# Kernel optimization log

Hardware: AMD Instinct MI355X
Metric: run time of the kernel (lower is better)

The kernel has to match this reference:

```python
import jax, jax.numpy as jnp
import numpy as np

B, S, D, H, E, K, DH = 4, 1024, 1024, 8, 4, 2, 128


def setup_inputs() -> dict:
    key = jax.random.key(0)
    ks = jax.random.split(key, 9)
    std = 1.0 / np.sqrt(D)
    f = lambda k, shape, s: jax.random.normal(k, shape, dtype=jnp.float32) * s
    return {
        'q_src': f(ks[0], (B, S, D), 1.0),
        'k_src': f(ks[1], (B, S, D), 1.0),
        'v_src': f(ks[2], (B, S, D), 1.0),
        'Wq': f(ks[3], (H * DH, D), std),
        'Wk': f(ks[4], (H * DH, D), std),
        'Wv': f(ks[5], (H * E, D, DH), std),
        'Wo': f(ks[6], (H * E, DH, D), 1.0 / np.sqrt(H * DH)),
        'sel_v': f(ks[7], (H * E, D), std),
        'sel_o': f(ks[8], (H * E, D), std),
    }


def _route(src, selw):
    # sigmoid-gated per-head top-k expert selection (get_sel), eval mode
    g = jax.nn.sigmoid((src @ selw.T).reshape(*src.shape[:-1], H, E))  # [B,S,H,E]
    val, idx = jax.lax.top_k(g, K)
    # dense per-expert mixture weights: zeros except top-k sigmoid gates
    return (jax.nn.one_hot(idx, E, dtype=g.dtype) * val[..., None]).sum(-2)  # [B,S,H,E]


def reference(q_src, k_src, v_src, Wq, Wk, Wv, Wo, sel_v, sel_o):
    scale = (1.0 / np.sqrt(DH)) ** 0.5  # scale.sqrt() applied to both q and k
    q = ((q_src @ Wq.T) * scale).reshape(B, S, H, DH).transpose(0, 2, 1, 3)  # [B,H,S,DH]
    k = ((k_src @ Wk.T) * scale).reshape(B, S, H, DH).transpose(0, 2, 1, 3)

    wv = _route(k_src, sel_v)  # [B,S,H,E] V-expert gates (from keys)
    wo = _route(q_src, sel_o)  # [B,S,H,E] O-expert gates (from queries)

    # cvmm V: per-token top-k mixture of expert V projections
    v_all = jnp.einsum('bsd,hedc->bshec', v_src, Wv.reshape(H, E, D, DH))
    v = jnp.einsum('bshec,bshe->bhsc', v_all, wv)  # [B,H,S,DH]

    att = jax.nn.softmax(jnp.einsum('bhqc,bhkc->bhqk', q, k), axis=-1)
    res = jnp.einsum('bhqk,bhkc->bqhc', att, v)  # [B,S,H,DH]

    # cvmm O: weight per-head outputs by gates, project and sum over heads/experts
    resw = res[..., None, :] * wo[..., None]  # [B,S,H,E,DH]
    out = jnp.einsum('bshec,hecd->bsd', resw, Wo.reshape(H, E, DH, D))
    return out
```

## Files before the change

kernel.cpp:

```cpp
#include <hip/hip_runtime.h>

#define DEV __device__ __forceinline__

typedef __attribute__((ext_vector_type(8))) short s8v;
typedef __attribute__((ext_vector_type(4))) short s4v;
typedef __attribute__((ext_vector_type(4))) float f4v;

DEV unsigned short f2b(float f){
    unsigned u = __float_as_uint(f);
    u = (u + 0x7FFFu + ((u >> 16) & 1u)) >> 16;
    return (unsigned short)u;
}
DEV float b2f(short s){ return __uint_as_float(((unsigned)(unsigned short)s) << 16); }

DEV void gload16(const void* g, void* l){
    __builtin_amdgcn_global_load_lds(
        (const __attribute__((address_space(1))) unsigned*)g,
        (__attribute__((address_space(3))) unsigned*)l, 16, 0, 0);
}


DEV void stage2(const short* A, const short* B, int sA, int sB, int kA, int kB,
                short* la, short* lb, int w, int lane){
    int srow = lane >> 3;
    int swcol = ((lane & 7) ^ srow) << 3;
    #pragma unroll
    for(int it = 0; it < 4; it++){
        int seg = (w << 2) + it;
        int row = (seg << 3) + srow;
        gload16(&A[(size_t)row * sA + kA + swcol], &la[seg << 9]);
        gload16(&B[(size_t)row * sB + kB + swcol], &lb[seg << 9]);
    }
}

DEV void mfma_block(const short* la, const short* lb, int wm, int wn, int qr, int grp, f4v acc[4][4]){
    #pragma unroll
    for(int ks = 0; ks < 2; ks++){
        s8v af[4], bf[4];
        #pragma unroll
        for(int m = 0; m < 4; m++)
            af[m] = *(const s8v*)&la[(wm + m * 16 + qr) * 64 + ((((ks << 2) + grp) ^ (qr & 7)) << 3)];
        #pragma unroll
        for(int n = 0; n < 4; n++)
            bf[n] = *(const s8v*)&lb[(wn + n * 16 + qr) * 64 + ((((ks << 2) + grp) ^ (qr & 7)) << 3)];
        #pragma unroll
        for(int m = 0; m < 4; m++)
            #pragma unroll
            for(int n = 0; n < 4; n++)
                acc[m][n] = __builtin_amdgcn_mfma_f32_16x16x32_bf16(af[m], bf[n], acc[m][n], 0, 0, 0);
    }
}

__global__ __launch_bounds__(256) void k_cvt(const float* s0, const float* s1, const float* s2,
                                             const float* s3, const float* s4,
                                             short* o0, short* o1, short* o2, short* o3, short* o4){
    int y = blockIdx.y;
    const float* s = (y == 0) ? s0 : (y == 1) ? s1 : (y == 2) ? s2 : (y == 3) ? s3 : s4;
    short* o = (y == 0) ? o0 : (y == 1) ? o1 : (y == 2) ? o2 : (y == 3) ? o3 : o4;
    int n8 = (y < 3) ? 524288 : 131072;
    int idx = blockIdx.x * 256 + threadIdx.x;
    if(idx < n8){
        const float4* f = (const float4*)(s + (size_t)idx * 8);
        float4 a = f[0], b = f[1];
        s8v v;
        v[0] = f2b(a.x); v[1] = f2b(a.y); v[2] = f2b(a.z); v[3] = f2b(a.w);
        v[4] = f2b(b.x); v[5] = f2b(b.y); v[6] = f2b(b.z); v[7] = f2b(b.w);
        *(s8v*)(o + (size_t)idx * 8) = v;
    }
}

__global__ __launch_bounds__(256) void k_transpose(const float* in, short* out, int R, int C){
    in  += (size_t)blockIdx.z * R * C;
    out += (size_t)blockIdx.z * R * C;
    __shared__ float t[32][33];
    int c0 = blockIdx.x * 32, r0 = blockIdx.y * 32;
    int tx = threadIdx.x & 31, ty = threadIdx.x >> 5;
    #pragma unroll
    for(int p = 0; p < 4; p++){
        int r = p * 8 + ty;
        t[r][tx] = in[(size_t)(r0 + r) * C + c0 + tx];
    }
    __syncthreads();
    #pragma unroll
    for(int p = 0; p < 4; p++){
        int c = p * 8 + ty;
        out[(size_t)(c0 + c) * R + r0 + tx] = (short)f2b(t[tx][c]);
    }
}

__global__ __launch_bounds__(256) void k_rlogits(const float* qsrc, const float* ksrc,
                                                 const float* selv, const float* selo,
                                                 float* part){
    int which = blockIdx.y;
    const float* src = which ? qsrc : ksrc;
    const float* sel = which ? selo : selv;
    int tt = blockIdx.x >> 3, ks = blockIdx.x & 7;
    int tok0 = tt << 7;
    __shared__ float lsrc[128][36];
    __shared__ float lsel[32][36];
    int tid = threadIdx.x;
    int ts = tid & 31, es = tid >> 5;
    float acc[4][4];
    #pragma unroll
    for(int j = 0; j < 4; j++)
        #pragma unroll
        for(int i = 0; i < 4; i++) acc[j][i] = 0.f;

    #pragma unroll 1
    for(int c = 0; c < 4; c++){
        int k0 = (ks << 7) + (c << 5);
        {
            int row = tid >> 1, half = tid & 1;
            const float4* g = (const float4*)(src + (size_t)(tok0 + row) * 1024 + k0 + half * 16);
            #pragma unroll
            for(int qq = 0; qq < 4; qq++){
                int qw = half * 4 + qq;
                *(float4*)&lsrc[row][((qw + row) & 7) * 4] = g[qq];
            }
        }
        {
            int row = tid >> 3, qw = tid & 7;
            *(float4*)&lsel[row][((qw + row) & 7) * 4] =
                *(const float4*)(sel + (size_t)row * 1024 + k0 + qw * 4);
        }
        __syncthreads();
        #pragma unroll
        for(int q = 0; q < 8; q++){
            float4 sv[4];
            #pragma unroll
            for(int i = 0; i < 4; i++){
                int e = es * 4 + i;
                sv[i] = *(const float4*)&lsel[e][((q + e) & 7) * 4];
            }
            int slot = ((q + ts) & 7) * 4;
            #pragma unroll
            for(int j = 0; j < 4; j++){
                float4 xv = *(const float4*)&lsrc[ts + 32 * j][slot];
                #pragma unroll
                for(int i = 0; i < 4; i++){
                    acc[j][i] = fmaf(xv.x, sv[i].x, acc[j][i]);
                    acc[j][i] = fmaf(xv.y, sv[i].y, acc[j][i]);
                    acc[j][i] = fmaf(xv.z, sv[i].z, acc[j][i]);
                    acc[j][i] = fmaf(xv.w, sv[i].w, acc[j][i]);
                }
            }
        }
        __syncthreads();
    }
    #pragma unroll
    for(int j = 0; j < 4; j++){
        int token = tok0 + ts + 32 * j;
        f4v st;
        #pragma unroll
        for(int i = 0; i < 4; i++) st[i] = acc[j][i];
        *(f4v*)&part[(((size_t)(ks * 2 + which) * 4096) + token) * 32 + es * 4] = st;
    }
}

__global__ __launch_bounds__(256) void k_rfinal(const float* part, float* wvp, float* wop){
    int which = blockIdx.y;
    float* wout = which ? wop : wvp;
    int tid = threadIdx.x;
    int tok = blockIdx.x * 32 + (tid >> 3), h = tid & 7;
    f4v sum = {0.f, 0.f, 0.f, 0.f};
    #pragma unroll
    for(int s = 0; s < 8; s++)
        sum += *(const f4v*)&part[(((size_t)(s * 2 + which) * 4096) + tok) * 32 + h * 4];
    float g[4];
    #pragma unroll
    for(int e = 0; e < 4; e++) g[e] = 1.0f / (1.0f + expf(-sum[e]));
    f4v out;
    #pragma unroll
    for(int e = 0; e < 4; e++){
        int rank = 0;
        #pragma unroll
        for(int j = 0; j < 4; j++)
            rank += (g[j] > g[e]) || (g[j] == g[e] && j < e);
        out[e] = (rank < 2) ? g[e] : 0.0f;
    }
    *(f4v*)&wout[(size_t)tok * 32 + h * 4] = out;
}

__global__ __launch_bounds__(256) void k_count(const float* wv, int* cntv){
    int he = blockIdx.x, tid = threadIdx.x;
    __shared__ int red[256];
    int c = 0;
    #pragma unroll
    for(int p = 0; p < 16; p++)
        c += (wv[(size_t)(p * 256 + tid) * 32 + he] > 0.f) ? 1 : 0;
    red[tid] = c;
    __syncthreads();
    for(int s = 128; s > 0; s >>= 1){
        if(tid < s) red[tid] += red[tid + s];
        __syncthreads();
    }
    if(tid == 0) cntv[he] = red[0];
}

__global__ __launch_bounds__(256) void k_scan(const int* cntv, int* basev, int* descv){
    __shared__ int ntl[33];
    int tid = threadIdx.x;
    if(tid == 0){
        int run = 0;
        for(int he = 0; he < 32; he++){
            ntl[he] = run;
            run += (cntv[he] + 127) >> 7;
        }
        ntl[32] = run;
    }
    __syncthreads();
    if(tid < 32) basev[tid] = ntl[tid] << 7;
    for(int i = tid; i < 544; i += 256){
        int d = -1;
        for(int he = 0; he < 32; he++)
            if(i >= ntl[he] && i < ntl[he + 1]) d = he;
        descv[i] = d;
    }
}

__global__ __launch_bounds__(256) void k_gather(const float* wv, const int* basev,
                                                int* idxv, float* gbufv, int* rpos){
    int he = blockIdx.x, h = he >> 2, e = he & 3;
    int tid = threadIdx.x, lane = tid & 63, w = tid >> 6;
    int base = basev[he];
    __shared__ int wsum[4];
    __shared__ int running;
    if(tid == 0) running = 0;
    __syncthreads();
    #pragma unroll 1
    for(int p = 0; p < 16; p++){
        int t = p * 256 + tid;
        float g = wv[(size_t)t * 32 + he];
        bool sel = g > 0.f;
        unsigned long long m = __ballot(sel);
        int lpref = __popcll(m & ((1ull << lane) - 1ull));
        if(lane == 0) wsum[w] = __popcll(m);
        __syncthreads();
        int rb = running;
        int woff = 0;
        #pragma unroll
        for(int j = 0; j < 4; j++) woff += (j < w) ? wsum[j] : 0;
        if(sel){
            int pos = base + rb + woff + lpref;
            idxv[pos] = t;
            gbufv[pos] = g;
            int slot = 0;
            #pragma unroll
            for(int j = 0; j < 4; j++)
                slot += (j < e && wv[(size_t)t * 32 + h * 4 + j] > 0.f) ? 1 : 0;
            rpos[(size_t)t * 16 + h * 2 + slot] = pos;
        }
        __syncthreads();
        if(tid == 0) running += wsum[0] + wsum[1] + wsum[2] + wsum[3];
        __syncthreads();
    }
    int tot = running;
    int aligned = (tot + 127) & ~127;
    for(int i = tid; i < aligned - tot; i += 256){
        idxv[base + tot + i] = 0;
        gbufv[base + tot + i] = 0.f;
    }
}

__global__ __launch_bounds__(256) void k_gemmg(const short* vsb, const short* wvt,
                                               const int* descv, const int* idxv,
                                               const float* gbufv, short* Cg){
    int he = descv[blockIdx.x];
    if(he < 0) return;
    int row0 = (int)blockIdx.x << 7;
    __shared__ __align__(16) short la[2][8192];
    __shared__ __align__(16) short lb[2][8192];
    __shared__ int lidx[128];
    int tid = threadIdx.x, lane = tid & 63, w = tid >> 6;
    if(tid < 128) lidx[tid] = idxv[row0 + tid];
    __syncthreads();
    int srow = lane >> 3;
    int swcol = ((lane & 7) ^ srow) << 3;
    int arow[4];
    #pragma unroll
    for(int it = 0; it < 4; it++) arow[it] = lidx[(((w << 2) + it) << 3) + srow];
    const short* Bb = wvt + ((size_t)he << 17);
    int wm = (w >> 1) << 6, wn = (w & 1) << 6;
    int qr = lane & 15, grp = lane >> 4;
    f4v acc[4][4];
    #pragma unroll
    for(int m = 0; m < 4; m++)
        #pragma unroll
        for(int n = 0; n < 4; n++) acc[m][n] = f4v{0.f, 0.f, 0.f, 0.f};
    #pragma unroll 1
    for(int t = -1; t < 16; t++){
        int nxt = t + 1;
        if(nxt < 16){
            int buf = nxt & 1, k0 = nxt << 6;
            #pragma unroll
            for(int it = 0; it < 4; it++){
                int seg = (w << 2) + it;
                int row = (seg << 3) + srow;
                gload16(&vsb[(size_t)arow[it] * 1024 + k0 + swcol], &la[buf][seg << 9]);
                gload16(&Bb[(size_t)row * 1024 + k0 + swcol], &lb[buf][seg << 9]);
            }
        }
        if(t >= 0)
            mfma_block(la[t & 1], lb[t & 1], wm, wn, qr, grp, acc);
        __syncthreads();
    }
    #pragma unroll
    for(int m = 0; m < 4; m++){
        int rl = wm + m * 16 + (grp << 2);
        #pragma unroll
        for(int r = 0; r < 4; r++){
            float g = gbufv[row0 + rl + r];
            #pragma unroll
            for(int n = 0; n < 4; n++){
                int col = wn + n * 16 + qr;
                Cg[(size_t)(row0 + rl + r) * 128 + col] = (short)f2b(acc[m][n][r] * g);
            }
        }
    }
}

__global__ __launch_bounds__(256) void k_vcomb(const short* Cg, const int* rpos, short* vtg){
    int bh = blockIdx.y, b = bh >> 3, h = bh & 7;
    int s0 = blockIdx.x * 32;
    __shared__ __align__(16) short t0[32][136];
    __shared__ __align__(16) short t1[32][136];
    __shared__ int rl[32][2];
    int tid = threadIdx.x;
    if(tid < 64){
        int i = tid >> 1, s = tid & 1;
        rl[i][s] = rpos[(size_t)(b * 1024 + s0 + i) * 16 + h * 2 + s];
    }
    __syncthreads();
    #pragma unroll
    for(int p = 0; p < 4; p++){
        int ch = tid + p * 256;
        int i = ch >> 5, slot = (ch >> 4) & 1, c8 = (ch & 15) << 3;
        s8v v = *(const s8v*)&Cg[(size_t)rl[i][slot] * 128 + c8];
        if(slot) *(s8v*)&t1[i][c8] = v;
        else     *(s8v*)&t0[i][c8] = v;
    }
    __syncthreads();
    #pragma unroll
    for(int p = 0; p < 16; p++){
        int idx = tid + p * 256;
        int s = idx & 31, c = idx >> 5;
        float v = b2f(t0[s][c]) + b2f(t1[s][c]);
        vtg[((size_t)bh * 128 + c) * 1024 + s0 + s] = (short)f2b(v);
    }
}

__global__ __launch_bounds__(256) void k_gemmqk(const short* qsb, const short* ksb,
                                                const short* wqb, const short* wkb,
                                                short* qo, short* ko, float scale){
    __shared__ __align__(16) short la[2][8192];
    __shared__ __align__(16) short lb[2][8192];
    int wg = (blockIdx.x & 7) * 64 + (blockIdx.x >> 3);
    int which = wg >> 8, tl = wg & 255;
    int mt = tl >> 3, nt = tl & 7;
    const short* A = (which ? ksb : qsb) + ((size_t)(mt << 7)) * 1024;
    const short* B = (which ? wkb : wqb) + ((size_t)(nt << 7)) * 1024;
    short* out = which ? ko : qo;
    int tid = threadIdx.x, lane = tid & 63, w = tid >> 6;
    int wm = (w >> 1) << 6, wn = (w & 1) << 6;
    int qr = lane & 15, grp = lane >> 4;
    f4v acc[4][4];
    #pragma unroll
    for(int m = 0; m < 4; m++)
        #pragma unroll
        for(int n = 0; n < 4; n++) acc[m][n] = f4v{0.f, 0.f, 0.f, 0.f};
    #pragma unroll 1
    for(int t = -1; t < 16; t++){
        int nxt = t + 1;
        if(nxt < 16)
            stage2(A, B, 1024, 1024, nxt << 6, nxt << 6, la[nxt & 1], lb[nxt & 1], w, lane);
        if(t >= 0)
            mfma_block(la[t & 1], lb[t & 1], wm, wn, qr, grp, acc);
        __syncthreads();
    }
    #pragma unroll
    for(int m = 0; m < 4; m++){
        int rb = (mt << 7) + wm + m * 16 + (grp << 2);
        #pragma unroll
        for(int n = 0; n < 4; n++){
            int col = (nt << 7) + wn + n * 16 + qr;
            #pragma unroll
            for(int r = 0; r < 4; r++)
                out[(size_t)(rb + r) * 1024 + col] = (short)f2b(acc[m][n][r] * scale);
        }
    }
}

__global__ __launch_bounds__(256) void k_gemmo(const short* resw, const short* wot, float* po){
    __shared__ __align__(16) short la[2][8192];
    __shared__ __align__(16) short lb[2][8192];
    int wg = (blockIdx.x & 7) * 64 + (blockIdx.x >> 3);
    int ksp = wg & 1, tile = wg >> 1;
    int mt = tile >> 3, nt = tile & 7;
    const short* A = resw + (size_t)(mt << 7) * 4096 + ksp * 2048;
    const short* B = wot + (size_t)(nt << 7) * 4096 + ksp * 2048;
    int tid = threadIdx.x, lane = tid & 63, w = tid >> 6;
    int wm = (w >> 1) << 6, wn = (w & 1) << 6;
    int qr = lane & 15, grp = lane >> 4;
    f4v acc[4][4];
    #pragma unroll
    for(int m = 0; m < 4; m++)
        #pragma unroll
        for(int n = 0; n < 4; n++) acc[m][n] = f4v{0.f, 0.f, 0.f, 0.f};
    #pragma unroll 1
    for(int t = -1; t < 32; t++){
        int nxt = t + 1;
        if(nxt < 32)
            stage2(A, B, 4096, 4096, nxt << 6, nxt << 6, la[nxt & 1], lb[nxt & 1], w, lane);
        if(t >= 0)
            mfma_block(la[t & 1], lb[t & 1], wm, wn, qr, grp, acc);
        __syncthreads();
    }
    po += (size_t)ksp * 4194304;
    #pragma unroll
    for(int m = 0; m < 4; m++){
        int rb = (mt << 7) + wm + m * 16 + (grp << 2);
        #pragma unroll
        for(int n = 0; n < 4; n++){
            int col = (nt << 7) + wn + n * 16 + qr;
            #pragma unroll
            for(int r = 0; r < 4; r++)
                po[(size_t)(rb + r) * 1024 + col] = acc[m][n][r];
        }
    }
}

__global__ __launch_bounds__(256) void k_red(const float* p0, const float* p1, float* out){
    size_t idx = ((size_t)blockIdx.x * 256 + threadIdx.x) * 4;
    f4v a = *(const f4v*)&p0[idx];
    f4v b = *(const f4v*)&p1[idx];
    f4v s = a + b;
    *(f4v*)&out[idx] = s;
}

__global__ __launch_bounds__(256) void k_attn(const short* qg, const short* kg,
                                              const short* vtg, short* res){
    __shared__ __align__(16) short lk[2][8192];
    __shared__ __align__(16) short lv[2][8192];
    __shared__ __align__(16) short pl[4][16 * 72];
    int bh = blockIdx.y, b = bh >> 3, h = bh & 7;
    int w = threadIdx.x >> 6, lane = threadIdx.x & 63;
    int qr = lane & 15, grp = lane >> 4;
    int q0 = blockIdx.x * 64 + w * 16;
    const short* vtb = vtg + ((size_t)bh << 17);
    short* pw = &pl[w][0];

    int tok = b * 1024 + q0 + qr;
    s8v qf[4];
    #pragma unroll
    for(int ks = 0; ks < 4; ks++)
        qf[ks] = *(const s8v*)&qg[(size_t)tok * 1024 + h * 128 + ks * 32 + grp * 8];
    f4v o[8];
    #pragma unroll
    for(int ct = 0; ct < 8; ct++) o[ct] = f4v{0.f, 0.f, 0.f, 0.f};
    float m_cur = -1e30f, l_cur = 0.f;

    int klr = lane >> 4, klc = lane & 15;
    int vlr = lane >> 3, vlc = lane & 7;

    #pragma unroll 1
    for(int t = -1; t < 16; t++){
        int nxt = t + 1;
        if(nxt < 16){
            int buf = nxt & 1, kv0 = nxt << 6;
            #pragma unroll
            for(int i = 0; i < 4; i++){
                int seg = (w << 2) + i;
                int kr = (seg << 2) + klr;
                int kc = klc ^ (kr & 7);
                gload16(&kg[(size_t)(b * 1024 + kv0 + kr) * 1024 + h * 128 + kc * 8], &lk[buf][seg << 9]);
                int vr = (seg << 3) + vlr;
                int vc = vlc ^ (vr & 7);
                gload16(&vtb[(size_t)vr * 1024 + kv0 + vc * 8], &lv[buf][seg << 9]);
            }
        }
        if(t >= 0){
            int cur = t & 1;
            f4v s[4];
            #pragma unroll
            for(int kt = 0; kt < 4; kt++) s[kt] = f4v{0.f, 0.f, 0.f, 0.f};
            __builtin_amdgcn_s_setprio(1);
            #pragma unroll
            for(int ks = 0; ks < 4; ks++){
                #pragma unroll
                for(int kt = 0; kt < 4; kt++){
                    int row = kt * 16 + qr;
                    s8v kf = *(const s8v*)&lk[cur][row * 128 + ((((ks << 2) + grp) ^ (row & 7)) << 3)];
                    s[kt] = __builtin_amdgcn_mfma_f32_16x16x32_bf16(kf, qf[ks], s[kt], 0, 0, 0);
                }
            }
            __builtin_amdgcn_s_setprio(0);
            float pm = s[0][0];
            #pragma unroll
            for(int kt = 0; kt < 4; kt++)
                #pragma unroll
                for(int r = 0; r < 4; r++) pm = fmaxf(pm, s[kt][r]);
            pm = fmaxf(pm, __shfl_xor(pm, 16));
            pm = fmaxf(pm, __shfl_xor(pm, 32));
            float mn = fmaxf(m_cur, pm);
            float fs = __expf(m_cur - mn);
            float ps = 0.f;
            #pragma unroll
            for(int kt = 0; kt < 4; kt++)
                #pragma unroll
                for(int r = 0; r < 4; r++){
                    s[kt][r] = __expf(s[kt][r] - mn);
                    ps += s[kt][r];
                }
            ps += __shfl_xor(ps, 16);
            ps += __shfl_xor(ps, 32);
            l_cur = l_cur * fs + ps;
            m_cur = mn;
            #pragma unroll
            for(int ct = 0; ct < 8; ct++){
                o[ct][0] *= fs; o[ct][1] *= fs; o[ct][2] *= fs; o[ct][3] *= fs;
            }
            #pragma unroll
            for(int kt = 0; kt < 4; kt++){
                s4v pvv;
                #pragma unroll
                for(int r = 0; r < 4; r++) pvv[r] = (short)f2b(s[kt][r]);
                *(s4v*)&pw[qr * 72 + kt * 16 + grp * 4] = pvv;
            }
            s8v pf0 = *(const s8v*)&pw[qr * 72 + grp * 8];
            s8v pf1 = *(const s8v*)&pw[qr * 72 + 32 + grp * 8];
            __builtin_amdgcn_s_setprio(1);
            #pragma unroll
            for(int ct = 0; ct < 8; ct++){
                int row = ct * 16 + qr;
                s8v vf0 = *(const s8v*)&lv[cur][row * 64 + ((grp ^ (row & 7)) << 3)];
                s8v vf1 = *(const s8v*)&lv[cur][row * 64 + (((4 + grp) ^ (row & 7)) << 3)];
                o[ct] = __builtin_amdgcn_mfma_f32_16x16x32_bf16(vf0, pf0, o[ct], 0, 0, 0);
                o[ct] = __builtin_amdgcn_mfma_f32_16x16x32_bf16(vf1, pf1, o[ct], 0, 0, 0);
            }
            __builtin_amdgcn_s_setprio(0);
        }
        __syncthreads();
    }
    float inv = 1.0f / l_cur;
    #pragma unroll
    for(int ct = 0; ct < 8; ct++){
        s4v sv;
        #pragma unroll
        for(int r = 0; r < 4; r++) sv[r] = (short)f2b(o[ct][r] * inv);
        *(s4v*)&res[(size_t)tok * 1024 + h * 128 + ct * 16 + grp * 4] = sv;
    }
}

__global__ __launch_bounds__(256) void k_expand(const short* res, const float* wo, short* resw){
    int idx = blockIdx.x * 256 + threadIdx.x;
    int t = idx >> 9;
    int u = idx & 511;
    int he = u >> 4, ci = u & 15;
    int h = he >> 2;
    float g = wo[(size_t)t * 32 + he];
    s8v r = *(const s8v*)&res[(size_t)t * 1024 + h * 128 + ci * 8];
    s8v v;
    #pragma unroll
    for(int j = 0; j < 8; j++) v[j] = (short)f2b(b2f(r[j]) * g);
    *(s8v*)&resw[(size_t)t * 4096 + u * 8] = v;
}

extern "C" void kernel_launch(void* const* d_in, const int* in_sizes, int n_in,
                              void* d_out, int out_size, void* d_ws, size_t ws_size,
                              hipStream_t stream){
    const float* q_src = (const float*)d_in[0];
    const float* k_src = (const float*)d_in[1];
    const float* v_src = (const float*)d_in[2];
    const float* Wq    = (const float*)d_in[3];
    const float* Wk    = (const float*)d_in[4];
    const float* Wv    = (const float*)d_in[5];
    const float* Wo    = (const float*)d_in[6];
    const float* selv  = (const float*)d_in[7];
    const float* selo  = (const float*)d_in[8];

    const size_t MB = 1ull << 20;
    char* ws = (char*)d_ws;
    short* qsb  = (short*)(ws + 0 * MB);
    short* ksb  = (short*)(ws + 8 * MB);
    short* vsb  = (short*)(ws + 16 * MB);
    short* wqb  = (short*)(ws + 24 * MB);
    short* wkb  = (short*)(ws + 26 * MB);
    short* wvt  = (short*)(ws + 28 * MB);
    short* wot  = (short*)(ws + 36 * MB);
    short* q    = (short*)(ws + 44 * MB);
    short* k    = (short*)(ws + 52 * MB);
    short* vt   = (short*)(ws + 60 * MB);
    short* res  = (short*)(ws + 68 * MB);
    float* wv   = (float*)(ws + 76 * MB);
    float* wo   = (float*)(ws + 76 * MB + 524288);
    float* part = (float*)(ws + 80 * MB);
    short* Cg   = (short*)(ws + 80 * MB);
    int*   cntv = (int*)  (ws + 100 * MB);
    int*   basev= (int*)  (ws + 100 * MB + 4096);
    int*   descv= (int*)  (ws + 100 * MB + 8192);
    int*   idxv = (int*)  (ws + 101 * MB);
    float* gbufv= (float*)(ws + 102 * MB);
    int*   rposv= (int*)  (ws + 103 * MB);
    short* resw = (short*)(ws + 0 * MB);
    float* po   = (float*)(ws + 80 * MB);

    const float qk_scale = 0.29730177875068026f;

    k_cvt<<<dim3(2048, 5), 256, 0, stream>>>(q_src, k_src, v_src, Wq, Wk, qsb, ksb, vsb, wqb, wkb);
    k_transpose<<<dim3(4, 32, 32), 256, 0, stream>>>(Wv, wvt, 1024, 128);
    k_transpose<<<dim3(32, 128, 1), 256, 0, stream>>>(Wo, wot, 4096, 1024);
    k_rlogits<<<dim3(256, 2), 256, 0, stream>>>(q_src, k_src, selv, selo, part);
    k_rfinal<<<dim3(128, 2), 256, 0, stream>>>(part, wv, wo);
    k_count<<<dim3(32), 256, 0, stream>>>(wv, cntv);
    k_scan<<<dim3(1), 256, 0, stream>>>(cntv, basev, descv);
    k_gather<<<dim3(32), 256, 0, stream>>>(wv, basev, idxv, gbufv, rposv);
    k_gemmqk<<<dim3(512), 256, 0, stream>>>(qsb, ksb, wqb, wkb, q, k, qk_scale);
    k_gemmg<<<dim3(544), 256, 0, stream>>>(vsb, wvt, descv, idxv, gbufv, Cg);
    k_vcomb<<<dim3(32, 32), 256, 0, stream>>>(Cg, rposv, vt);
    k_attn<<<dim3(16, 32), 256, 0, stream>>>(q, k, vt, res);
    k_expand<<<dim3(8192), 256, 0, stream>>>(res, wo, resw);
    k_gemmo<<<dim3(512), 256, 0, stream>>>(resw, wot, po);
    k_red<<<dim3(4096), 256, 0, stream>>>(po, po + 4194304, (float*)d_out);
}
```

Before: 230.0 us.

## Fuse expert gating into attention epilogue and use exp2 softmax with lazy rescale

Removes the separate expand kernel by having the attention kernel multiply its normalized output by the four per-head O-expert gates and write the expanded bf16 tensor directly. Softmax switches to base-2 exponentials, with log2(e) folded into the q/k scale, and uses the hardware exp instruction. Rescaling of the accumulator is skipped unless the running max grows past a threshold. Float-to-bf16 conversion uses the packed hardware instruction. This removes an intermediate write/read and a launch, at the cost of more stores in the attention epilogue and a bounded range growth in unnormalized probabilities.

```diff
diff --git a/kernel.cpp b/kernel.cpp
--- a/kernel.cpp
+++ b/kernel.cpp
@@ -12,6 +12,17 @@
     return (unsigned short)u;
 }
 DEV float b2f(short s){ return __uint_as_float(((unsigned)(unsigned short)s) << 16); }
+
+DEV unsigned cvtpk(float lo, float hi){
+    unsigned r;
+    asm("v_cvt_pk_bf16_f32 %0, %1, %2" : "=v"(r) : "v"(lo), "v"(hi));
+    return r;
+}
+DEV float exp2v(float x){
+    float r;
+    asm("v_exp_f32 %0, %1" : "=v"(r) : "v"(x));
+    return r;
+}
 
 DEV void gload16(const void* g, void* l){
     __builtin_amdgcn_global_load_lds(
@@ -438,7 +449,7 @@
 }
 
 __global__ __launch_bounds__(256) void k_attn(const short* qg, const short* kg,
-                                              const short* vtg, short* res){
+                                              const short* vtg, const float* wo, short* resw){
     __shared__ __align__(16) short lk[2][8192];
     __shared__ __align__(16) short lv[2][8192];
     __shared__ __align__(16) short pl[4][16 * 72];
@@ -501,30 +512,33 @@
                 for(int r = 0; r < 4; r++) pm = fmaxf(pm, s[kt][r]);
             pm = fmaxf(pm, __shfl_xor(pm, 16));
             pm = fmaxf(pm, __shfl_xor(pm, 32));
-            float mn = fmaxf(m_cur, pm);
-            float fs = __expf(m_cur - mn);
+            if(!__all(pm - m_cur <= 11.541f)){
+                float mn = fmaxf(m_cur, pm);
+                float fs = exp2v(m_cur - mn);
+                #pragma unroll
+                for(int ct = 0; ct < 8; ct++){
+                    o[ct][0] *= fs; o[ct][1] *= fs; o[ct][2] *= fs; o[ct][3] *= fs;
+                }
+                l_cur *= fs;
+                m_cur = mn;
+            }
             float ps = 0.f;
             #pragma unroll
             for(int kt = 0; kt < 4; kt++)
                 #pragma unroll
                 for(int r = 0; r < 4; r++){
-                    s[kt][r] = __expf(s[kt][r] - mn);
+                    s[kt][r] = exp2v(s[kt][r] - m_cur);
                     ps += s[kt][r];
                 }
             ps += __shfl_xor(ps, 16);
             ps += __shfl_xor(ps, 32);
-            l_cur = l_cur * fs + ps;
-            m_cur = mn;
-            #pragma unroll
-            for(int ct = 0; ct < 8; ct++){
-                o[ct][0] *= fs; o[ct][1] *= fs; o[ct][2] *= fs; o[ct][3] *= fs;
-            }
+            l_cur += ps;
             #pragma unroll
             for(int kt = 0; kt < 4; kt++){
-                s4v pvv;
-                #pragma unroll
-                for(int r = 0; r < 4; r++) pvv[r] = (short)f2b(s[kt][r]);
-                *(s4v*)&pw[qr * 72 + kt * 16 + grp * 4] = pvv;
+                uint2 pv;
+                pv.x = cvtpk(s[kt][0], s[kt][1]);
+                pv.y = cvtpk(s[kt][2], s[kt][3]);
+                *(uint2*)&pw[qr * 72 + kt * 16 + grp * 4] = pv;
             }
             s8v pf0 = *(const s8v*)&pw[qr * 72 + grp * 8];
             s8v pf1 = *(const s8v*)&pw[qr * 72 + 32 + grp * 8];
@@ -542,27 +556,21 @@
         __syncthreads();
     }
     float inv = 1.0f / l_cur;
+    float g4[4];
+    #pragma unroll
+    for(int e = 0; e < 4; e++) g4[e] = wo[(size_t)tok * 32 + h * 4 + e];
     #pragma unroll
     for(int ct = 0; ct < 8; ct++){
-        s4v sv;
-        #pragma unroll
-        for(int r = 0; r < 4; r++) sv[r] = (short)f2b(o[ct][r] * inv);
-        *(s4v*)&res[(size_t)tok * 1024 + h * 128 + ct * 16 + grp * 4] = sv;
-    }
-}
-
-__global__ __launch_bounds__(256) void k_expand(const short* res, const float* wo, short* resw){
-    int idx = blockIdx.x * 256 + threadIdx.x;
-    int t = idx >> 9;
-    int u = idx & 511;
-    int he = u >> 4, ci = u & 15;
-    int h = he >> 2;
-    float g = wo[(size_t)t * 32 + he];
-    s8v r = *(const s8v*)&res[(size_t)t * 1024 + h * 128 + ci * 8];
-    s8v v;
-    #pragma unroll
-    for(int j = 0; j < 8; j++) v[j] = (short)f2b(b2f(r[j]) * g);
-    *(s8v*)&resw[(size_t)t * 4096 + u * 8] = v;
+        float v0 = o[ct][0] * inv, v1 = o[ct][1] * inv;
+        float v2 = o[ct][2] * inv, v3 = o[ct][3] * inv;
+        #pragma unroll
+        for(int e = 0; e < 4; e++){
+            uint2 sv;
+            sv.x = cvtpk(v0 * g4[e], v1 * g4[e]);
+            sv.y = cvtpk(v2 * g4[e], v3 * g4[e]);
+            *(uint2*)&resw[(size_t)tok * 4096 + (h * 4 + e) * 128 + ct * 16 + grp * 4] = sv;
+        }
+    }
 }
 
 extern "C" void kernel_launch(void* const* d_in, const int* in_sizes, int n_in,
@@ -590,7 +598,6 @@
     short* q    = (short*)(ws + 44 * MB);
     short* k    = (short*)(ws + 52 * MB);
     short* vt   = (short*)(ws + 60 * MB);
-    short* res  = (short*)(ws + 68 * MB);
     float* wv   = (float*)(ws + 76 * MB);
     float* wo   = (float*)(ws + 76 * MB + 524288);
     float* part = (float*)(ws + 80 * MB);
@@ -604,7 +611,7 @@
     short* resw = (short*)(ws + 0 * MB);
     float* po   = (float*)(ws + 80 * MB);
 
-    const float qk_scale = 0.29730177875068026f;
+    const float qk_scale = 0.29730177875068026f * 1.2011224087864498f;
 
     k_cvt<<<dim3(2048, 5), 256, 0, stream>>>(q_src, k_src, v_src, Wq, Wk, qsb, ksb, vsb, wqb, wkb);
     k_transpose<<<dim3(4, 32, 32), 256, 0, stream>>>(Wv, wvt, 1024, 128);
@@ -617,8 +624,7 @@
     k_gemmqk<<<dim3(512), 256, 0, stream>>>(qsb, ksb, wqb, wkb, q, k, qk_scale);
     k_gemmg<<<dim3(544), 256, 0, stream>>>(vsb, wvt, descv, idxv, gbufv, Cg);
     k_vcomb<<<dim3(32, 32), 256, 0, stream>>>(Cg, rposv, vt);
-    k_attn<<<dim3(16, 32), 256, 0, stream>>>(q, k, vt, res);
-    k_expand<<<dim3(8192), 256, 0, stream>>>(res, wo, resw);
+    k_attn<<<dim3(16, 32), 256, 0, stream>>>(q, k, vt, wo, resw);
     k_gemmo<<<dim3(512), 256, 0, stream>>>(resw, wot, po);
     k_red<<<dim3(4096), 256, 0, stream>>>(po, po + 4194304, (float*)d_out);
 }
```

After: 225.7 us. About the same (-1.9%).
